# Kernel tuning notes

Measured on AMD Instinct MI355X. Metric: run time of the kernel, lower is better.

## Reference

```python
import jax, jax.numpy as jnp
import numpy as np

B = 4096          # graph pairs in batch
NPG = 40          # nodes per molecular graph
N = B * NPG       # total nodes per drug batch
EPG = 160         # directed edges per graph
E = B * EPG
F_IN = 78         # atom feature dim
HID = 128
HEADS = 4
ADD = 8           # additional features (concentrations)
BN_EPS = 1e-5
D0 = HEADS * HID          # 512
CMB = 4 * HID + ADD       # 2 drugs * (mean||max of 128) + ADD = 520


def setup_inputs() -> dict:
    key = jax.random.key(0)
    ks = iter(jax.random.split(key, 64))
    def nrm(shape, s=0.1):
        return jax.random.normal(next(ks), shape, jnp.float32) * s
    def pos(shape):  # positive running variances
        return jax.random.uniform(next(ks), shape, jnp.float32, 0.5, 1.5)
    offs = jnp.repeat(jnp.arange(B, dtype=jnp.int32) * NPG, EPG)
    def edges():
        return jax.random.randint(next(ks), (2, E), 0, NPG, dtype=jnp.int32) + offs[None, :]
    batch = jnp.repeat(jnp.arange(B, dtype=jnp.int32), NPG)
    inp = dict(
        x_a=nrm((N, F_IN), 1.0), edge_a=edges(), batch_a=batch,
        x_b=nrm((N, F_IN), 1.0), edge_b=edges(), batch_b=batch,
        addf=nrm((B, ADD), 1.0),
        # shared GAT encoder params
        gW0=nrm((F_IN, D0)), gb0=nrm((D0,)), gas0=nrm((D0,)), gad0=nrm((D0,)),
        gW1=nrm((D0, D0)), gb1=nrm((D0,)), gas1=nrm((D0,)), gad1=nrm((D0,)),
        gW2=nrm((D0, HID)), gb2=nrm((HID,)), gas2=nrm((HID,)), gad2=nrm((HID,)),
        bn0g=pos((D0,)), bn0b=nrm((D0,)), bn0m=nrm((D0,)), bn0v=pos((D0,)),
        bn1g=pos((D0,)), bn1b=nrm((D0,)), bn1m=nrm((D0,)), bn1v=pos((D0,)),
        bn2g=pos((HID,)), bn2b=nrm((HID,)), bn2m=nrm((HID,)), bn2v=pos((HID,)),
        # combination MLP params (Linear + eval BatchNorm stats)
        mW0=nrm((CMB, 2 * HID)), mb0=nrm((2 * HID,)),
        mg0=pos((2 * HID,)), mbe0=nrm((2 * HID,)), mm0=nrm((2 * HID,)), mv0=pos((2 * HID,)),
        mW1=nrm((2 * HID, HID)), mb1=nrm((HID,)),
        mg1=pos((HID,)), mbe1=nrm((HID,)), mm1=nrm((HID,)), mv1=pos((HID,)),
        mW2=nrm((HID, 1)), mb2=nrm((1,)),
    )
    return inp


def _bn(x, g, b, m, v):
    return (x - m) * jax.lax.rsqrt(v + BN_EPS) * g + b


def _gat(x, src, dst, W, b, a_src, a_dst, heads, ch, concat):
    """PyG GATConv (eval): linear, per-head additive attention with
    leaky_relu(0.2), segment-softmax over incoming edges (self-loops included)."""
    n = x.shape[0]
    h = (x @ W).reshape(n, heads, ch)                     # [N, H, C]
    es = jnp.sum(h * a_src.reshape(1, heads, ch), -1)     # [N, H]
    ed = jnp.sum(h * a_dst.reshape(1, heads, ch), -1)     # [N, H]
    e = jax.nn.leaky_relu(es[src] + ed[dst], 0.2)         # [E', H]
    emax = jax.ops.segment_max(e, dst, num_segments=n)
    ex = jnp.exp(e - emax[dst])
    den = jax.ops.segment_sum(ex, dst, num_segments=n)
    alpha = ex / den[dst]                                 # [E', H]
    out = jax.ops.segment_sum(h[src] * alpha[..., None], dst, num_segments=n)
    out = out.reshape(n, heads * ch) if concat else jnp.mean(out, axis=1)
    return out + b


def _encode(x, edge, batch, p):
    n = x.shape[0]
    sl = jnp.arange(n, dtype=edge.dtype)                  # self-loops (PyG default)
    src = jnp.concatenate([edge[0], sl])
    dst = jnp.concatenate([edge[1], sl])
    x = _gat(x, src, dst, p['gW0'], p['gb0'], p['gas0'], p['gad0'], HEADS, HID, True)
    x = jax.nn.relu(_bn(x, p['bn0g'], p['bn0b'], p['bn0m'], p['bn0v']))
    x = _gat(x, src, dst, p['gW1'], p['gb1'], p['gas1'], p['gad1'], HEADS, HID, True)
    x = jax.nn.relu(_bn(x, p['bn1g'], p['bn1b'], p['bn1m'], p['bn1v']))
    x = _gat(x, src, dst, p['gW2'], p['gb2'], p['gas2'], p['gad2'], 1, HID, False)
    x = _bn(x, p['bn2g'], p['bn2b'], p['bn2m'], p['bn2v'])  # no relu on last layer
    cnt = jax.ops.segment_sum(jnp.ones((n, 1), x.dtype), batch, num_segments=B)
    x_mean = jax.ops.segment_sum(x, batch, num_segments=B) / cnt
    x_max = jax.ops.segment_max(x, batch, num_segments=B)
    return jnp.concatenate([x_mean, x_max], axis=1)        # [B, 2*HID]


def reference(x_a, edge_a, batch_a, x_b, edge_b, batch_b, addf,
              gW0, gb0, gas0, gad0, gW1, gb1, gas1, gad1, gW2, gb2, gas2, gad2,
              bn0g, bn0b, bn0m, bn0v, bn1g, bn1b, bn1m, bn1v, bn2g, bn2b, bn2m, bn2v,
              mW0, mb0, mg0, mbe0, mm0, mv0, mW1, mb1, mg1, mbe1, mm1, mv1, mW2, mb2):
    p = dict(gW0=gW0, gb0=gb0, gas0=gas0, gad0=gad0, gW1=gW1, gb1=gb1, gas1=gas1,
             gad1=gad1, gW2=gW2, gb2=gb2, gas2=gas2, gad2=gad2,
             bn0g=bn0g, bn0b=bn0b, bn0m=bn0m, bn0v=bn0v,
             bn1g=bn1g, bn1b=bn1b, bn1m=bn1m, bn1v=bn1v,
             bn2g=bn2g, bn2b=bn2b, bn2m=bn2m, bn2v=bn2v)
    emb_a = _encode(x_a, edge_a, batch_a, p)
    emb_b = _encode(x_b, edge_b, batch_b, p)
    c = jnp.concatenate([emb_a, emb_b, addf], axis=1)      # [B, 520]
    h = jax.nn.relu(_bn(c @ mW0 + mb0, mg0, mbe0, mm0, mv0))
    h = jax.nn.relu(_bn(h @ mW1 + mb1, mg1, mbe1, mm1, mv1))
    out = jax.nn.sigmoid(h @ mW2 + mb2)
    return jnp.squeeze(out, -1)                            # [B]
```

## Files before the change

kernel.cpp:

```cpp
#include <hip/hip_runtime.h>
#include <stdint.h>

#define B_GRAPHS 4096
#define NPG 40
#define NTOT (B_GRAPHS * NPG)
#define EPG 160
#define ETOT (B_GRAPHS * EPG)
#define ESL 200
#define F_IN 78
#define KP0 96
#define HID 128
#define D0 512
#define CMB 520
#define BN_EPS 1e-5f
#define AST 48
#define KPM 544
#define A0ST 552
#define H1ST 264
#define H2ST 132

typedef short bf16x8 __attribute__((ext_vector_type(8)));
typedef float floatx4 __attribute__((ext_vector_type(4)));

__device__ inline float b2f(unsigned short u) {
    union { float f; uint32_t i; } v; v.i = ((uint32_t)u) << 16; return v.f;
}
__device__ inline unsigned short f2b(float f) {
    union { float f; uint32_t i; } v; v.f = f;
    uint32_t x = v.i;
    return (unsigned short)((x + 0x7fffu + ((x >> 16) & 1u)) >> 16);
}
__device__ inline float lo16(uint32_t u) {
    union { float f; uint32_t i; } v; v.i = u << 16; return v.f;
}
__device__ inline float hi16(uint32_t u) {
    union { float f; uint32_t i; } v; v.i = u & 0xffff0000u; return v.f;
}
__device__ inline unsigned int fenc(float f) {
    unsigned int b = __float_as_uint(f);
    return (b & 0x80000000u) ? ~b : (b | 0x80000000u);
}
__device__ inline float fdec(unsigned int u) {
    unsigned int b = (u & 0x80000000u) ? (u & 0x7fffffffu) : ~u;
    return __uint_as_float(b);
}
__device__ inline int htoff(int ch, int s) {
    int chunk = s >> 3, within = s & 7;
    return ch * 40 + (((chunk + ch) % 5) << 3) + within;
}
__device__ inline void gl2lds16(const unsigned short* g, unsigned short* l) {
    __builtin_amdgcn_global_load_lds(
        (const __attribute__((address_space(1))) unsigned int*)g,
        (__attribute__((address_space(3))) unsigned int*)l, 16, 0, 0);
}

__global__ __launch_bounds__(256)
void write_code_kernel(float* __restrict__ out, int n, float S)
{
    int i = blockIdx.x * 256 + threadIdx.x;
    if (i < n) out[i] = (i == 0) ? S : 0.f;
}

__global__ __launch_bounds__(256)
void convw_kernel(const float* __restrict__ W, unsigned short* __restrict__ Wt,
                  int K, int N, int Kp)
{
    int t = blockIdx.x * 256 + threadIdx.x;
    if (t >= N * Kp) return;
    int n = t / Kp, k = t - n * Kp;
    Wt[t] = (k < K) ? f2b(W[(size_t)k * N + n]) : 0;
}

__global__ __launch_bounds__(256)
void convw_hilo_kernel(const float* __restrict__ W,
                       unsigned short* __restrict__ Whi,
                       unsigned short* __restrict__ Wlo,
                       int K, int N, int Kp)
{
    int t = blockIdx.x * 256 + threadIdx.x;
    if (t >= N * Kp) return;
    int n = t / Kp, k = t - n * Kp;
    float x = (k < K) ? W[(size_t)k * N + n] : 0.f;
    unsigned short hb = f2b(x);
    Whi[t] = hb;
    Wlo[t] = f2b(x - b2f(hb));
}

__global__ __launch_bounds__(256)
void convx_kernel(const float* __restrict__ X, unsigned short* __restrict__ Xb, int M)
{
    int t = blockIdx.x * 256 + threadIdx.x;
    if (t >= M * (KP0 / 8)) return;
    int r = t / (KP0 / 8), c8 = t - r * (KP0 / 8);
    unsigned int pk[4];
    #pragma unroll
    for (int j = 0; j < 4; j++) {
        int k0 = c8 * 8 + 2 * j, k1 = k0 + 1;
        float x0 = (k0 < F_IN) ? X[(size_t)r * F_IN + k0] : 0.f;
        float x1 = (k1 < F_IN) ? X[(size_t)r * F_IN + k1] : 0.f;
        pk[j] = (unsigned int)f2b(x0) | ((unsigned int)f2b(x1) << 16);
    }
    *(uint4*)&Xb[(size_t)r * KP0 + c8 * 8] = make_uint4(pk[0], pk[1], pk[2], pk[3]);
}

__global__ __launch_bounds__(256)
void gemm_mfma_kernel(const unsigned short* __restrict__ A,
                      const unsigned short* __restrict__ Bt,
                      unsigned short* __restrict__ C,
                      int M, int K, int N)
{
    __shared__ __align__(16) unsigned short As[128 * 32];
    __shared__ __align__(16) unsigned short Bs[128 * 32];
    const int tid  = threadIdx.x;
    const int lane = tid & 63, w = tid >> 6;
    const int quad = lane >> 4, l16 = lane & 15;
    const int wm = w >> 1, wn = w & 1;
    const int row0 = blockIdx.y * 128, col0 = blockIdx.x * 128;

    floatx4 acc[4][4];
    #pragma unroll
    for (int mi = 0; mi < 4; mi++)
        #pragma unroll
        for (int ni = 0; ni < 4; ni++)
            acc[mi][ni] = (floatx4){0.f, 0.f, 0.f, 0.f};

    int srow[2], scg[2];
    #pragma unroll
    for (int it = 0; it < 2; it++) {
        int L = it * 4096 + w * 1024 + lane * 16;
        int r = L >> 6;
        int cp = (L >> 4) & 3;
        srow[it] = r;
        scg[it]  = cp ^ ((r >> 1) & 3);
    }

    for (int k0 = 0; k0 < K; k0 += 32) {
        #pragma unroll
        for (int it = 0; it < 2; it++) {
            int ra = row0 + srow[it]; if (ra >= M) ra = M - 1;
            gl2lds16(A + (size_t)ra * K + k0 + scg[it] * 8,
                     As + (it * 4096 + w * 1024) / 2);
            int rb = col0 + srow[it];
            gl2lds16(Bt + (size_t)rb * K + k0 + scg[it] * 8,
                     Bs + (it * 4096 + w * 1024) / 2);
        }
        __syncthreads();

        bf16x8 fA[4], fB[4];
        #pragma unroll
        for (int mi = 0; mi < 4; mi++) {
            int r = wm * 64 + mi * 16 + l16;
            __builtin_memcpy(&fA[mi], &As[r * 32 + ((quad ^ ((r >> 1) & 3)) * 8)], 16);
        }
        #pragma unroll
        for (int ni = 0; ni < 4; ni++) {
            int r = wn * 64 + ni * 16 + l16;
            __builtin_memcpy(&fB[ni], &Bs[r * 32 + ((quad ^ ((r >> 1) & 3)) * 8)], 16);
        }
        #pragma unroll
        for (int mi = 0; mi < 4; mi++)
            #pragma unroll
            for (int ni = 0; ni < 4; ni++)
                acc[mi][ni] = __builtin_amdgcn_mfma_f32_16x16x32_bf16(
                    fB[ni], fA[mi], acc[mi][ni], 0, 0, 0);
        __syncthreads();
    }

    #pragma unroll
    for (int mi = 0; mi < 4; mi++) {
        int row = row0 + wm * 64 + mi * 16 + l16;
        if (row < M) {
            #pragma unroll
            for (int ni = 0; ni < 4; ni++) {
                floatx4 a = acc[mi][ni];
                unsigned int p0 = (unsigned int)f2b(a[0]) | ((unsigned int)f2b(a[1]) << 16);
                unsigned int p1 = (unsigned int)f2b(a[2]) | ((unsigned int)f2b(a[3]) << 16);
                *(uint2*)(C + (size_t)row * N + col0 + wn * 64 + ni * 16 + quad * 4) =
                    make_uint2(p0, p1);
            }
        }
    }
}

__global__ __launch_bounds__(256)
void gat4_fused_kernel(unsigned short* __restrict__ H,
                       const int* __restrict__ edge,
                       const float* __restrict__ avs, const float* __restrict__ avd,
                       const float* __restrict__ bias,
                       const float* __restrict__ bng, const float* __restrict__ bnb,
                       const float* __restrict__ bnm, const float* __restrict__ bnv,
                       int g0)
{
    __shared__ __align__(16) unsigned short ht[D0 * NPG];
    __shared__ float es[4 * NPG], ed[4 * NPG];
    __shared__ unsigned int Mu[4 * NPG];
    __shared__ float den[4 * NPG];
    __shared__ __align__(16) unsigned char cnt[NPG * 48];
    __shared__ short2 eloc[ESL];
    const int tid = threadIdx.x;
    const int lane = tid & 63, w = tid >> 6;
    const int quad = lane >> 4, l16 = lane & 15;
    const int gg = g0 + blockIdx.x;
    unsigned short* Hg = H + (size_t)blockIdx.x * NPG * D0;

    for (int i = tid; i < NPG * 48 / 4; i += 256) ((unsigned int*)cnt)[i] = 0u;
    if (tid < 4 * NPG) { Mu[tid] = 0u; den[tid] = 0.f; }
    for (int i = tid; i < ESL; i += 256) {
        if (i < EPG) {
            int s  = edge[(size_t)gg * EPG + i] - gg * NPG;
            int dd = edge[(size_t)ETOT + (size_t)gg * EPG + i] - gg * NPG;
            eloc[i] = make_short2((short)s, (short)dd);
        } else {
            short v = (short)(i - EPG);
            eloc[i] = make_short2(v, v);
        }
    }
    for (int u = tid; u < 64 * (NPG / 4); u += 256) {
        int c8 = u & 63, gi = u >> 6;
        const unsigned short* src = Hg + (size_t)(4 * gi) * D0 + c8 * 8;
        uint4 v0 = *(const uint4*)(src);
        uint4 v1 = *(const uint4*)(src + D0);
        uint4 v2 = *(const uint4*)(src + 2 * D0);
        uint4 v3 = *(const uint4*)(src + 3 * D0);
        unsigned int a0[4] = {v0.x, v0.y, v0.z, v0.w};
        unsigned int a1[4] = {v1.x, v1.y, v1.z, v1.w};
        unsigned int a2[4] = {v2.x, v2.y, v2.z, v2.w};
        unsigned int a3[4] = {v3.x, v3.y, v3.z, v3.w};
        #pragma unroll
        for (int k = 0; k < 8; k++) {
            const int ws = k >> 1, sh = (k & 1) * 16;
            unsigned int w0 = ((a0[ws] >> sh) & 0xffffu) | (((a1[ws] >> sh) & 0xffffu) << 16);
            unsigned int w1 = ((a2[ws] >> sh) & 0xffffu) | (((a3[ws] >> sh) & 0xffffu) << 16);
            *(uint2*)&ht[htoff(c8 * 8 + k, 4 * gi)] = make_uint2(w0, w1);
        }
    }
    __syncthreads();

    {
        float as0=0,as1=0,as2=0,as3=0, ad0=0,ad1=0,ad2=0,ad3=0;
        for (int ci = 0; ci < 32; ci++) {
            int c = quad + ci * 4;
            int chv = w * 128 + c;
            uint2 hv = *(const uint2*)&ht[htoff(chv, 4 * l16)];
            float h0 = lo16(hv.x), h1 = hi16(hv.x), h2 = lo16(hv.y), h3 = hi16(hv.y);
            float vs = avs[chv], vd = avd[chv];
            as0 += h0*vs; as1 += h1*vs; as2 += h2*vs; as3 += h3*vs;
            ad0 += h0*vd; ad1 += h1*vd; ad2 += h2*vd; ad3 += h3*vd;
        }
        #define RED4(x) x += __shfl_xor(x, 16); x += __shfl_xor(x, 32);
        RED4(as0) RED4(as1) RED4(as2) RED4(as3)
        RED4(ad0) RED4(ad1) RED4(ad2) RED4(ad3)
        #undef RED4
        if (quad == 0) {
            float rs[4] = {as0, as1, as2, as3};
            float rd[4] = {ad0, ad1, ad2, ad3};
            #pragma unroll
            for (int rr = 0; rr < 4; rr++) {
                int node = 4 * l16 + rr;
                if (node < NPG) { es[w * NPG + node] = rs[rr]; ed[w * NPG + node] = rd[rr]; }
            }
        }
    }
    for (int e = tid; e < ESL; e += 256) {
        short2 sd = eloc[e];
        atomicAdd((unsigned int*)cnt + ((sd.y * 48 + sd.x) >> 2),
                  1u << ((sd.x & 3) * 8));
    }
    __syncthreads();

    for (int u = tid; u < 4 * ESL; u += 256) {
        int e = u >> 2, hd = u & 3;
        short2 sd = eloc[e];
        float v = es[hd * NPG + sd.x] + ed[hd * NPG + sd.y];
        v = v > 0.f ? v : 0.2f * v;
        atomicMax(&Mu[hd * NPG + sd.y], fenc(v));
    }
    __syncthreads();
    for (int u = tid; u < 4 * ESL; u += 256) {
        int e = u >> 2, hd = u & 3;
        short2 sd = eloc[e];
        float v = es[hd * NPG + sd.x] + ed[hd * NPG + sd.y];
        v = v > 0.f ? v : 0.2f * v;
        float ex = __expf(v - fdec(Mu[hd * NPG + sd.y]));
        atomicAdd(&den[hd * NPG + sd.y], ex);
    }
    __syncthreads();
// ... 36 lines not shown
                unsigned short hb1 = f2b(a1);
                ahi[mt][1][j] = (short)hb1;
                alo[mt][1][j] = (short)f2b(a1 - b2f(hb1));
            }
        }
        const floatx4 z = {0.f, 0.f, 0.f, 0.f};
        for (int nt = 0; nt < 8; nt++) {
            const int ch0 = w * 128 + nt * 16;
            bf16x8 b0, b1 = {0,0,0,0,0,0,0,0};
            __builtin_memcpy(&b0, &ht[htoff(ch0 + l16, quad * 8)], 16);
            if (quad == 0) __builtin_memcpy(&b1, &ht[htoff(ch0 + l16, 32)], 16);
            floatx4 acc0 = z, acc1 = z, acc2 = z;
            acc0 = __builtin_amdgcn_mfma_f32_16x16x32_bf16(ahi[0][0], b0, acc0, 0, 0, 0);
            acc1 = __builtin_amdgcn_mfma_f32_16x16x32_bf16(ahi[1][0], b0, acc1, 0, 0, 0);
            acc2 = __builtin_amdgcn_mfma_f32_16x16x32_bf16(ahi[2][0], b0, acc2, 0, 0, 0);
            acc0 = __builtin_amdgcn_mfma_f32_16x16x32_bf16(alo[0][0], b0, acc0, 0, 0, 0);
            acc1 = __builtin_amdgcn_mfma_f32_16x16x32_bf16(alo[1][0], b0, acc1, 0, 0, 0);
            acc2 = __builtin_amdgcn_mfma_f32_16x16x32_bf16(alo[2][0], b0, acc2, 0, 0, 0);
            acc0 = __builtin_amdgcn_mfma_f32_16x16x32_bf16(ahi[0][1], b1, acc0, 0, 0, 0);
            acc1 = __builtin_amdgcn_mfma_f32_16x16x32_bf16(ahi[1][1], b1, acc1, 0, 0, 0);
            acc2 = __builtin_amdgcn_mfma_f32_16x16x32_bf16(ahi[2][1], b1, acc2, 0, 0, 0);
            acc0 = __builtin_amdgcn_mfma_f32_16x16x32_bf16(alo[0][1], b1, acc0, 0, 0, 0);
            acc1 = __builtin_amdgcn_mfma_f32_16x16x32_bf16(alo[1][1], b1, acc1, 0, 0, 0);
            acc2 = __builtin_amdgcn_mfma_f32_16x16x32_bf16(alo[2][1], b1, acc2, 0, 0, 0);
            const int c = ch0 + l16;
            float scl = rsqrtf(bnv[c] + BN_EPS) * bng[c];
            float sft = (bias[c] - bnm[c]) * scl + bnb[c];
            unsigned short* reg = &ht[ch0 * 40];
            #pragma unroll
            for (int mt = 0; mt < 3; mt++) {
                floatx4 a = (mt == 0) ? acc0 : (mt == 1) ? acc1 : acc2;
                #pragma unroll
                for (int rr = 0; rr < 4; rr++) {
                    int dn = mt * 16 + quad * 4 + rr;
                    if (dn < NPG) {
                        float o = a[rr] * scl + sft;
                        o = fmaxf(o, 0.f);
                        reg[dn * 16 + l16] = f2b(o);
                    }
                }
            }
        }
    }
    __syncthreads();
    for (int u = tid; u < NPG * 64; u += 256) {
        int s = u >> 6, c8 = u & 63;
        const unsigned short* reg = &ht[(c8 >> 1) * 16 * 40];
        uint4 v = *(const uint4*)&reg[s * 16 + (c8 & 1) * 8];
        *(uint4*)(Hg + (size_t)s * D0 + c8 * 8) = v;
    }
}

__global__ __launch_bounds__(256)
void gat1_pool_fused_kernel(const unsigned short* __restrict__ H,
                            const int* __restrict__ edge,
                            const float* __restrict__ avs, const float* __restrict__ avd,
                            const float* __restrict__ bias,
                            const float* __restrict__ bng, const float* __restrict__ bnb,
                            const float* __restrict__ bnm, const float* __restrict__ bnv,
                            float* __restrict__ cmb, int colbase, int g0)
{
    __shared__ __align__(16) unsigned short ht[HID * NPG];
    __shared__ float A1f[NPG * AST];
    __shared__ float es[NPG], ed[NPG];
    __shared__ unsigned int Mu[NPG];
    __shared__ float den[NPG];
    __shared__ short2 eloc[ESL];
    const int tid = threadIdx.x;
    const int lane = tid & 63, w = tid >> 6;
    const int quad = lane >> 4, l16 = lane & 15;
    const int gg = g0 + blockIdx.x;
    const unsigned short* Hg = H + (size_t)blockIdx.x * NPG * HID;

    for (int i = tid; i < NPG * AST; i += 256) A1f[i] = 0.f;
    if (tid < NPG) { Mu[tid] = 0u; den[tid] = 0.f; }
    for (int i = tid; i < ESL; i += 256) {
        if (i < EPG) {
            int s  = edge[(size_t)gg * EPG + i] - gg * NPG;
            int dd = edge[(size_t)ETOT + (size_t)gg * EPG + i] - gg * NPG;
            eloc[i] = make_short2((short)s, (short)dd);
        } else {
            short v = (short)(i - EPG);
            eloc[i] = make_short2(v, v);
        }
    }
    for (int u = tid; u < 16 * (NPG / 4); u += 256) {
        int c8 = u & 15, gi = u >> 4;
        const unsigned short* src = Hg + (size_t)(4 * gi) * HID + c8 * 8;
        uint4 v0 = *(const uint4*)(src);
        uint4 v1 = *(const uint4*)(src + HID);
        uint4 v2 = *(const uint4*)(src + 2 * HID);
        uint4 v3 = *(const uint4*)(src + 3 * HID);
        unsigned int a0[4] = {v0.x, v0.y, v0.z, v0.w};
        unsigned int a1[4] = {v1.x, v1.y, v1.z, v1.w};
        unsigned int a2[4] = {v2.x, v2.y, v2.z, v2.w};
        unsigned int a3[4] = {v3.x, v3.y, v3.z, v3.w};
        #pragma unroll
        for (int k = 0; k < 8; k++) {
            const int ws = k >> 1, sh = (k & 1) * 16;
            unsigned int w0 = ((a0[ws] >> sh) & 0xffffu) | (((a1[ws] >> sh) & 0xffffu) << 16);
            unsigned int w1 = ((a2[ws] >> sh) & 0xffffu) | (((a3[ws] >> sh) & 0xffffu) << 16);
            *(uint2*)&ht[htoff(c8 * 8 + k, 4 * gi)] = make_uint2(w0, w1);
        }
    }
    __syncthreads();

    if (w < 2) {
        const float* av = w ? avd : avs;
        float a0=0,a1=0,a2=0,a3=0;
        for (int ci = 0; ci < 32; ci++) {
            int c = quad + ci * 4;
            uint2 hv = *(const uint2*)&ht[htoff(c, 4 * l16)];
            float vc = av[c];
            a0 += lo16(hv.x)*vc; a1 += hi16(hv.x)*vc;
            a2 += lo16(hv.y)*vc; a3 += hi16(hv.y)*vc;
        }
        #define RED4(x) x += __shfl_xor(x, 16); x += __shfl_xor(x, 32);
        RED4(a0) RED4(a1) RED4(a2) RED4(a3)
        #undef RED4
        if (quad == 0) {
            float rv[4] = {a0, a1, a2, a3};
            float* dst = w ? ed : es;
            #pragma unroll
            for (int rr = 0; rr < 4; rr++) {
                int node = 4 * l16 + rr;
                if (node < NPG) dst[node] = rv[rr];
            }
        }
    }
    __syncthreads();
    for (int u = tid; u < ESL; u += 256) {
        short2 sd = eloc[u];
        float v = es[sd.x] + ed[sd.y];
        v = v > 0.f ? v : 0.2f * v;
        atomicMax(&Mu[sd.y], fenc(v));
    }
    __syncthreads();
    for (int u = tid; u < ESL; u += 256) {
        short2 sd = eloc[u];
        float v = es[sd.x] + ed[sd.y];
        v = v > 0.f ? v : 0.2f * v;
        float ex = __expf(v - fdec(Mu[sd.y]));
        atomicAdd(&den[sd.y], ex);
        atomicAdd(&A1f[sd.x * AST + sd.y], ex);
    }
    __syncthreads();
    for (int idx = tid; idx < NPG * AST; idx += 256) {
        int dn = idx % AST;
        float val = A1f[idx];
        unsigned int pw = 0u;
        if (dn < NPG) {
            float a = val / den[dn];
            unsigned short hi = f2b(a);
            float rem = a - b2f(hi);
            pw = (unsigned int)hi | ((unsigned int)f2b(rem) << 16);
        }
        ((unsigned int*)A1f)[idx] = pw;
    }
    __syncthreads();

    {
        const unsigned int* Ap = (const unsigned int*)A1f;
        bf16x8 ahi[3][2], alo[3][2];
        #pragma unroll
        for (int mt = 0; mt < 3; mt++) {
            #pragma unroll
            for (int j = 0; j < 8; j++) {
                unsigned int w0 = Ap[(quad * 8 + j) * AST + mt * 16 + l16];
                ahi[mt][0][j] = (short)(w0 & 0xffffu);
                alo[mt][0][j] = (short)(w0 >> 16);
                unsigned int w1 = (quad == 0) ? Ap[(32 + j) * AST + mt * 16 + l16] : 0u;
                ahi[mt][1][j] = (short)(w1 & 0xffffu);
                alo[mt][1][j] = (short)(w1 >> 16);
            }
        }
        const floatx4 z = {0.f, 0.f, 0.f, 0.f};
        for (int t2 = 0; t2 < 2; t2++) {
            const int ch0 = (w * 2 + t2) * 16;
            bf16x8 b0, b1 = {0,0,0,0,0,0,0,0};
            __builtin_memcpy(&b0, &ht[htoff(ch0 + l16, quad * 8)], 16);
            if (quad == 0) __builtin_memcpy(&b1, &ht[htoff(ch0 + l16, 32)], 16);
            floatx4 acc0 = z, acc1 = z, acc2 = z;
            acc0 = __builtin_amdgcn_mfma_f32_16x16x32_bf16(ahi[0][0], b0, acc0, 0, 0, 0);
            acc1 = __builtin_amdgcn_mfma_f32_16x16x32_bf16(ahi[1][0], b0, acc1, 0, 0, 0);
            acc2 = __builtin_amdgcn_mfma_f32_16x16x32_bf16(ahi[2][0], b0, acc2, 0, 0, 0);
            acc0 = __builtin_amdgcn_mfma_f32_16x16x32_bf16(alo[0][0], b0, acc0, 0, 0, 0);
            acc1 = __builtin_amdgcn_mfma_f32_16x16x32_bf16(alo[1][0], b0, acc1, 0, 0, 0);
            acc2 = __builtin_amdgcn_mfma_f32_16x16x32_bf16(alo[2][0], b0, acc2, 0, 0, 0);
            acc0 = __builtin_amdgcn_mfma_f32_16x16x32_bf16(ahi[0][1], b1, acc0, 0, 0, 0);
            acc1 = __builtin_amdgcn_mfma_f32_16x16x32_bf16(ahi[1][1], b1, acc1, 0, 0, 0);
            acc2 = __builtin_amdgcn_mfma_f32_16x16x32_bf16(ahi[2][1], b1, acc2, 0, 0, 0);
            acc0 = __builtin_amdgcn_mfma_f32_16x16x32_bf16(alo[0][1], b1, acc0, 0, 0, 0);
            acc1 = __builtin_amdgcn_mfma_f32_16x16x32_bf16(alo[1][1], b1, acc1, 0, 0, 0);
            acc2 = __builtin_amdgcn_mfma_f32_16x16x32_bf16(alo[2][1], b1, acc2, 0, 0, 0);
            const int c = ch0 + l16;
            float scl = rsqrtf(bnv[c] + BN_EPS) * bng[c];
            float sft = (bias[c] - bnm[c]) * scl + bnb[c];
            float psum = 0.f, pmax = -1e30f;
            #pragma unroll
            for (int mt = 0; mt < 3; mt++) {
                floatx4 a = (mt == 0) ? acc0 : (mt == 1) ? acc1 : acc2;
                #pragma unroll
                for (int rr = 0; rr < 4; rr++) {
                    int dn = mt * 16 + quad * 4 + rr;
                    if (dn < NPG) {
                        float o = a[rr] * scl + sft;
                        psum += o;
                        pmax = fmaxf(pmax, o);
                    }
                }
            }
            psum += __shfl_xor(psum, 16); psum += __shfl_xor(psum, 32);
            pmax = fmaxf(pmax, __shfl_xor(pmax, 16));
            pmax = fmaxf(pmax, __shfl_xor(pmax, 32));
            if (quad == 0) {
                cmb[(size_t)gg * 512 + colbase + c] = psum * (1.f / NPG);
                cmb[(size_t)gg * 512 + colbase + HID + c] = pmax;
            }
        }
    }
}

__global__ __launch_bounds__(256)
void mlp_mfma_kernel(const float* __restrict__ cmb, const float* __restrict__ addf,
                     const unsigned short* __restrict__ W0hi, const unsigned short* __restrict__ W0lo,
                     const float* __restrict__ b0, const float* __restrict__ g0v,
// ... 107 lines not shown
        float s = 0.f;
        #pragma unroll
        for (int j = 0; j < 8; j++)
            s += h2[g * H2ST + part * 8 + j] * W2[part * 8 + j];
        s += __shfl_xor(s, 1); s += __shfl_xor(s, 2);
        s += __shfl_xor(s, 4); s += __shfl_xor(s, 8);
        if (part == 0) out[gb + g] = 1.f / (1.f + __expf(-(s + b2[0])));
    }
}

extern "C" void kernel_launch(void* const* d_in, const int* in_sizes, int n_in,
                              void* d_out, int out_size, void* d_ws, size_t ws_size,
                              hipStream_t stream)
{
    float* out = (float*)d_out;
    int out_n = out_size < 4096 ? out_size : 4096;

    const float* x_a  = (const float*)d_in[0];
    const int*   edge_a = (const int*)d_in[1];
    const float* x_b  = (const float*)d_in[3];
    const int*   edge_b = (const int*)d_in[4];
    const float* addf = (const float*)d_in[6];
    const float* gW0 = (const float*)d_in[7],  *gb0 = (const float*)d_in[8];
    const float* gas0 = (const float*)d_in[9], *gad0 = (const float*)d_in[10];
    const float* gW1 = (const float*)d_in[11], *gb1 = (const float*)d_in[12];
    const float* gas1 = (const float*)d_in[13], *gad1 = (const float*)d_in[14];
    const float* gW2 = (const float*)d_in[15], *gb2 = (const float*)d_in[16];
    const float* gas2 = (const float*)d_in[17], *gad2 = (const float*)d_in[18];
    const float* bn0g = (const float*)d_in[19], *bn0b = (const float*)d_in[20];
    const float* bn0m = (const float*)d_in[21], *bn0v = (const float*)d_in[22];
    const float* bn1g = (const float*)d_in[23], *bn1b = (const float*)d_in[24];
    const float* bn1m = (const float*)d_in[25], *bn1v = (const float*)d_in[26];
    const float* bn2g = (const float*)d_in[27], *bn2b = (const float*)d_in[28];
    const float* bn2m = (const float*)d_in[29], *bn2v = (const float*)d_in[30];
    const float* mW0 = (const float*)d_in[31], *mb0 = (const float*)d_in[32];
    const float* mg0 = (const float*)d_in[33], *mbe0 = (const float*)d_in[34];
    const float* mm0 = (const float*)d_in[35], *mv0 = (const float*)d_in[36];
    const float* mW1 = (const float*)d_in[37], *mb1 = (const float*)d_in[38];
    const float* mg1 = (const float*)d_in[39], *mbe1 = (const float*)d_in[40];
    const float* mm1 = (const float*)d_in[41], *mv1 = (const float*)d_in[42];
    const float* mW2 = (const float*)d_in[43], *mb2 = (const float*)d_in[44];

    char* p = (char*)d_ws;
    const size_t CMB_BYTES = (size_t)B_GRAPHS * 512 * sizeof(float);
    float* cmb = (float*)p; p += CMB_BYTES;
    unsigned short* W0t = (unsigned short*)p; p += (size_t)D0 * KP0 * 2;
    unsigned short* W1t = (unsigned short*)p; p += (size_t)D0 * D0 * 2;
    unsigned short* W2t = (unsigned short*)p; p += (size_t)HID * D0 * 2;
    unsigned short* M0hi = (unsigned short*)p; p += (size_t)256 * KPM * 2;
    unsigned short* M0lo = (unsigned short*)p; p += (size_t)256 * KPM * 2;
    unsigned short* M1hi = (unsigned short*)p; p += (size_t)128 * 256 * 2;
    unsigned short* M1lo = (unsigned short*)p; p += (size_t)128 * 256 * 2;
    size_t used = (size_t)(p - (char*)d_ws);
    const size_t PG = 7680ull + 40960ull + 40960ull;
    int chunk = B_GRAPHS;
    while (chunk > 4 && used + (size_t)chunk * PG > ws_size) chunk >>= 1;
    if (used + (size_t)chunk * PG > ws_size) {
        write_code_kernel<<<(out_n + 255) / 256, 256, 0, stream>>>(out, out_n, 500000.f);
        return;
    }
    unsigned short* Xb = (unsigned short*)p; p += (size_t)chunk * 7680;
    unsigned short* B1 = (unsigned short*)p; p += (size_t)chunk * 40960;
    unsigned short* B2 = (unsigned short*)p;

    convw_kernel<<<(D0 * KP0 + 255) / 256, 256, 0, stream>>>(gW0, W0t, F_IN, D0, KP0);
    convw_kernel<<<(D0 * D0 + 255) / 256, 256, 0, stream>>>(gW1, W1t, D0, D0, D0);
    convw_kernel<<<(HID * D0 + 255) / 256, 256, 0, stream>>>(gW2, W2t, D0, HID, D0);
    convw_hilo_kernel<<<(256 * KPM + 255) / 256, 256, 0, stream>>>(
        mW0, M0hi, M0lo, CMB, 256, KPM);
    convw_hilo_kernel<<<(128 * 256 + 255) / 256, 256, 0, stream>>>(
        mW1, M1hi, M1lo, 256, 128, 256);

    for (int drug = 0; drug < 2; drug++) {
        const float* x = drug ? x_b : x_a;
        const int* edge = drug ? edge_b : edge_a;
        int colbase = drug ? 256 : 0;

        for (int g0 = 0; g0 < B_GRAPHS; g0 += chunk) {
            int n = chunk * NPG;
            int gy = (n + 127) / 128;
            convx_kernel<<<(n * (KP0 / 8) + 255) / 256, 256, 0, stream>>>(
                x + (size_t)g0 * NPG * F_IN, Xb, n);
            gemm_mfma_kernel<<<dim3(D0 / 128, gy), 256, 0, stream>>>(
                Xb, W0t, B1, n, KP0, D0);
            gat4_fused_kernel<<<chunk, 256, 0, stream>>>(
                B1, edge, gas0, gad0, gb0, bn0g, bn0b, bn0m, bn0v, g0);
            gemm_mfma_kernel<<<dim3(D0 / 128, gy), 256, 0, stream>>>(
                B1, W1t, B2, n, D0, D0);
            gat4_fused_kernel<<<chunk, 256, 0, stream>>>(
                B2, edge, gas1, gad1, gb1, bn1g, bn1b, bn1m, bn1v, g0);
            gemm_mfma_kernel<<<dim3(HID / 128, gy), 256, 0, stream>>>(
                B2, W2t, B1, n, D0, HID);
            gat1_pool_fused_kernel<<<chunk, 256, 0, stream>>>(
                B1, edge, gas2, gad2, gb2, bn2g, bn2b, bn2m, bn2v,
                cmb, colbase, g0);
        }
    }
    mlp_mfma_kernel<<<B_GRAPHS / 16, 256, 0, stream>>>(
        cmb, addf, M0hi, M0lo, mb0, mg0, mbe0, mm0, mv0,
        M1hi, M1lo, mb1, mg1, mbe1, mm1, mv1, mW2, mb2, out);
}
```

Measured before the change: 1.419 ms.

## Fuse layer-0 and layer-2 GEMMs into per-graph GAT kernels

Layer 0 now does the bf16 conversion of raw float features and the X·W0 MFMA GEMM inside the per-graph GAT kernel, writing results straight to shared memory. This removes the convx kernel, the Xb buffer and one global round-trip of the 512-wide hidden tensor. Layer 2 likewise folds the 512→128 GEMM into the pooling GAT kernel. That kernel also switches from a float shared attention matrix built with atomics to a count matrix plus on-the-fly exp coefficients, as the 4-head kernel already does. In exchange, each block rereads the W0/W2 weights from global or L2, and the layer-0 feature loads are uncoalesced scalar loads with heavy register use (launch bound set to 3 blocks).

```diff
diff --git a/kernel.cpp b/kernel.cpp
--- a/kernel.cpp
+++ b/kernel.cpp
@@ -13,7 +13,6 @@
 #define D0 512
 #define CMB 520
 #define BN_EPS 1e-5f
-#define AST 48
 #define KPM 544
 #define A0ST 552
 #define H1ST 264
@@ -87,23 +86,6 @@
 }
 
 __global__ __launch_bounds__(256)
-void convx_kernel(const float* __restrict__ X, unsigned short* __restrict__ Xb, int M)
-{
-    int t = blockIdx.x * 256 + threadIdx.x;
-    if (t >= M * (KP0 / 8)) return;
-    int r = t / (KP0 / 8), c8 = t - r * (KP0 / 8);
-    unsigned int pk[4];
-    #pragma unroll
-    for (int j = 0; j < 4; j++) {
-        int k0 = c8 * 8 + 2 * j, k1 = k0 + 1;
-        float x0 = (k0 < F_IN) ? X[(size_t)r * F_IN + k0] : 0.f;
-        float x1 = (k1 < F_IN) ? X[(size_t)r * F_IN + k1] : 0.f;
-        pk[j] = (unsigned int)f2b(x0) | ((unsigned int)f2b(x1) << 16);
-    }
-    *(uint4*)&Xb[(size_t)r * KP0 + c8 * 8] = make_uint4(pk[0], pk[1], pk[2], pk[3]);
-}
-
-__global__ __launch_bounds__(256)
 void gemm_mfma_kernel(const unsigned short* __restrict__ A,
                       const unsigned short* __restrict__ Bt,
                       unsigned short* __restrict__ C,
@@ -182,14 +164,16 @@
     }
 }
 
-__global__ __launch_bounds__(256)
-void gat4_fused_kernel(unsigned short* __restrict__ H,
-                       const int* __restrict__ edge,
-                       const float* __restrict__ avs, const float* __restrict__ avd,
-                       const float* __restrict__ bias,
-                       const float* __restrict__ bng, const float* __restrict__ bnb,
-                       const float* __restrict__ bnm, const float* __restrict__ bnv,
-                       int g0)
+__global__ __launch_bounds__(256, 3)
+void fused0_kernel(const float* __restrict__ X,
+                   const unsigned short* __restrict__ Wt,
+                   unsigned short* __restrict__ Hout,
+                   const int* __restrict__ edge,
+                   const float* __restrict__ avs, const float* __restrict__ avd,
+                   const float* __restrict__ bias,
+                   const float* __restrict__ bng, const float* __restrict__ bnb,
+                   const float* __restrict__ bnm, const float* __restrict__ bnv,
+                   int g0)
 {
     __shared__ __align__(16) unsigned short ht[D0 * NPG];
     __shared__ float es[4 * NPG], ed[4 * NPG];
@@ -201,7 +185,8 @@
     const int lane = tid & 63, w = tid >> 6;
     const int quad = lane >> 4, l16 = lane & 15;
     const int gg = g0 + blockIdx.x;
-    unsigned short* Hg = H + (size_t)blockIdx.x * NPG * D0;
+    const float* Xg = X + (size_t)blockIdx.x * NPG * F_IN;
+    unsigned short* Hg = Hout + (size_t)blockIdx.x * NPG * D0;
 
     for (int i = tid; i < NPG * 48 / 4; i += 256) ((unsigned int*)cnt)[i] = 0u;
     if (tid < 4 * NPG) { Mu[tid] = 0u; den[tid] = 0.f; }
@@ -215,23 +200,51 @@
             eloc[i] = make_short2(v, v);
         }
     }
-    for (int u = tid; u < 64 * (NPG / 4); u += 256) {
-        int c8 = u & 63, gi = u >> 6;
-        const unsigned short* src = Hg + (size_t)(4 * gi) * D0 + c8 * 8;
-        uint4 v0 = *(const uint4*)(src);
-        uint4 v1 = *(const uint4*)(src + D0);
-        uint4 v2 = *(const uint4*)(src + 2 * D0);
-        uint4 v3 = *(const uint4*)(src + 3 * D0);
-        unsigned int a0[4] = {v0.x, v0.y, v0.z, v0.w};
-        unsigned int a1[4] = {v1.x, v1.y, v1.z, v1.w};
-        unsigned int a2[4] = {v2.x, v2.y, v2.z, v2.w};
-        unsigned int a3[4] = {v3.x, v3.y, v3.z, v3.w};
-        #pragma unroll
-        for (int k = 0; k < 8; k++) {
-            const int ws = k >> 1, sh = (k & 1) * 16;
-            unsigned int w0 = ((a0[ws] >> sh) & 0xffffu) | (((a1[ws] >> sh) & 0xffffu) << 16);
-            unsigned int w1 = ((a2[ws] >> sh) & 0xffffu) | (((a3[ws] >> sh) & 0xffffu) << 16);
-            *(uint2*)&ht[htoff(c8 * 8 + k, 4 * gi)] = make_uint2(w0, w1);
+
+    {
+        floatx4 acc[3][8];
+        #pragma unroll
+        for (int mt = 0; mt < 3; mt++)
+            #pragma unroll
+            for (int nt = 0; nt < 8; nt++)
+                acc[mt][nt] = (floatx4){0.f, 0.f, 0.f, 0.f};
+        #pragma unroll
+        for (int k0 = 0; k0 < KP0; k0 += 32) {
+            bf16x8 fA[3];
+            #pragma unroll
+            for (int mt = 0; mt < 3; mt++) {
+                int s = mt * 16 + l16; if (s >= NPG) s = NPG - 1;
+                const float* xr = Xg + (size_t)s * F_IN;
+                #pragma unroll
+                for (int j = 0; j < 8; j++) {
+                    int k = k0 + quad * 8 + j;
+                    float xv = (k < F_IN) ? xr[k] : 0.f;
+                    fA[mt][j] = (short)f2b(xv);
+                }
+            }
+            #pragma unroll
+            for (int nt = 0; nt < 8; nt++) {
+                int ch = w * 128 + nt * 16 + l16;
+                bf16x8 fW;
+                __builtin_memcpy(&fW, Wt + (size_t)ch * KP0 + k0 + quad * 8, 16);
+                acc[0][nt] = __builtin_amdgcn_mfma_f32_16x16x32_bf16(fA[0], fW, acc[0][nt], 0, 0, 0);
+                acc[1][nt] = __builtin_amdgcn_mfma_f32_16x16x32_bf16(fA[1], fW, acc[1][nt], 0, 0, 0);
+                acc[2][nt] = __builtin_amdgcn_mfma_f32_16x16x32_bf16(fA[2], fW, acc[2][nt], 0, 0, 0);
+            }
+        }
+        #pragma unroll
+        for (int nt = 0; nt < 8; nt++) {
+            int ch = w * 128 + nt * 16 + l16;
+            #pragma unroll
+            for (int mt = 0; mt < 3; mt++) {
+                int s0 = mt * 16 + quad * 4;
+                if (s0 < NPG) {
+                    floatx4 a = acc[mt][nt];
+                    unsigned int p0 = (unsigned int)f2b(a[0]) | ((unsigned int)f2b(a[1]) << 16);
+                    unsigned int p1 = (unsigned int)f2b(a[2]) | ((unsigned int)f2b(a[3]) << 16);
+                    *(uint2*)&ht[htoff(ch, s0)] = make_uint2(p0, p1);
+                }
+            }
         }
     }
     __syncthreads();
@@ -374,27 +387,219 @@
 }
 
 __global__ __launch_bounds__(256)
-void gat1_pool_fused_kernel(const unsigned short* __restrict__ H,
-                            const int* __restrict__ edge,
-                            const float* __restrict__ avs, const float* __restrict__ avd,
-                            const float* __restrict__ bias,
-                            const float* __restrict__ bng, const float* __restrict__ bnb,
-                            const float* __restrict__ bnm, const float* __restrict__ bnv,
-                            float* __restrict__ cmb, int colbase, int g0)
+void gat4_fused_kernel(unsigned short* __restrict__ H,
+                       const int* __restrict__ edge,
+                       const float* __restrict__ avs, const float* __restrict__ avd,
+                       const float* __restrict__ bias,
+                       const float* __restrict__ bng, const float* __restrict__ bnb,
+                       const float* __restrict__ bnm, const float* __restrict__ bnv,
+                       int g0)
 {
-    __shared__ __align__(16) unsigned short ht[HID * NPG];
-    __shared__ float A1f[NPG * AST];
-    __shared__ float es[NPG], ed[NPG];
-    __shared__ unsigned int Mu[NPG];
-    __shared__ float den[NPG];
+    __shared__ __align__(16) unsigned short ht[D0 * NPG];
+    __shared__ float es[4 * NPG], ed[4 * NPG];
+    __shared__ unsigned int Mu[4 * NPG];
+    __shared__ float den[4 * NPG];
+    __shared__ __align__(16) unsigned char cnt[NPG * 48];
     __shared__ short2 eloc[ESL];
     const int tid = threadIdx.x;
     const int lane = tid & 63, w = tid >> 6;
     const int quad = lane >> 4, l16 = lane & 15;
     const int gg = g0 + blockIdx.x;
-    const unsigned short* Hg = H + (size_t)blockIdx.x * NPG * HID;
-
-    for (int i = tid; i < NPG * AST; i += 256) A1f[i] = 0.f;
+    unsigned short* Hg = H + (size_t)blockIdx.x * NPG * D0;
+
+    for (int i = tid; i < NPG * 48 / 4; i += 256) ((unsigned int*)cnt)[i] = 0u;
+    if (tid < 4 * NPG) { Mu[tid] = 0u; den[tid] = 0.f; }
+    for (int i = tid; i < ESL; i += 256) {
+        if (i < EPG) {
+            int s  = edge[(size_t)gg * EPG + i] - gg * NPG;
+            int dd = edge[(size_t)ETOT + (size_t)gg * EPG + i] - gg * NPG;
+            eloc[i] = make_short2((short)s, (short)dd);
+        } else {
+            short v = (short)(i - EPG);
+            eloc[i] = make_short2(v, v);
+        }
+    }
+    for (int u = tid; u < 64 * (NPG / 4); u += 256) {
+        int c8 = u & 63, gi = u >> 6;
+        const unsigned short* src = Hg + (size_t)(4 * gi) * D0 + c8 * 8;
+        uint4 v0 = *(const uint4*)(src);
+        uint4 v1 = *(const uint4*)(src + D0);
+        uint4 v2 = *(const uint4*)(src + 2 * D0);
+        uint4 v3 = *(const uint4*)(src + 3 * D0);
+        unsigned int a0[4] = {v0.x, v0.y, v0.z, v0.w};
+        unsigned int a1[4] = {v1.x, v1.y, v1.z, v1.w};
+        unsigned int a2[4] = {v2.x, v2.y, v2.z, v2.w};
+        unsigned int a3[4] = {v3.x, v3.y, v3.z, v3.w};
+        #pragma unroll
+        for (int k = 0; k < 8; k++) {
+            const int ws = k >> 1, sh = (k & 1) * 16;
+            unsigned int w0 = ((a0[ws] >> sh) & 0xffffu) | (((a1[ws] >> sh) & 0xffffu) << 16);
+            unsigned int w1 = ((a2[ws] >> sh) & 0xffffu) | (((a3[ws] >> sh) & 0xffffu) << 16);
+            *(uint2*)&ht[htoff(c8 * 8 + k, 4 * gi)] = make_uint2(w0, w1);
+        }
+    }
+    __syncthreads();
+
+    {
+        float as0=0,as1=0,as2=0,as3=0, ad0=0,ad1=0,ad2=0,ad3=0;
+        for (int ci = 0; ci < 32; ci++) {
+            int c = quad + ci * 4;
+            int chv = w * 128 + c;
+            uint2 hv = *(const uint2*)&ht[htoff(chv, 4 * l16)];
+            float h0 = lo16(hv.x), h1 = hi16(hv.x), h2 = lo16(hv.y), h3 = hi16(hv.y);
+            float vs = avs[chv], vd = avd[chv];
+            as0 += h0*vs; as1 += h1*vs; as2 += h2*vs; as3 += h3*vs;
+            ad0 += h0*vd; ad1 += h1*vd; ad2 += h2*vd; ad3 += h3*vd;
+        }
+        #define RED4(x) x += __shfl_xor(x, 16); x += __shfl_xor(x, 32);
+        RED4(as0) RED4(as1) RED4(as2) RED4(as3)
+        RED4(ad0) RED4(ad1) RED4(ad2) RED4(ad3)
+        #undef RED4
+        if (quad == 0) {
+            float rs[4] = {as0, as1, as2, as3};
+            float rd[4] = {ad0, ad1, ad2, ad3};
+            #pragma unroll
+            for (int rr = 0; rr < 4; rr++) {
+                int node = 4 * l16 + rr;
+                if (node < NPG) { es[w * NPG + node] = rs[rr]; ed[w * NPG + node] = rd[rr]; }
+            }
+        }
+    }
+    for (int e = tid; e < ESL; e += 256) {
+        short2 sd = eloc[e];
+        atomicAdd((unsigned int*)cnt + ((sd.y * 48 + sd.x) >> 2),
+                  1u << ((sd.x & 3) * 8));
+    }
+    __syncthreads();
+
+    for (int u = tid; u < 4 * ESL; u += 256) {
+        int e = u >> 2, hd = u & 3;
+        short2 sd = eloc[e];
+        float v = es[hd * NPG + sd.x] + ed[hd * NPG + sd.y];
+        v = v > 0.f ? v : 0.2f * v;
+        atomicMax(&Mu[hd * NPG + sd.y], fenc(v));
+    }
+    __syncthreads();
+    for (int u = tid; u < 4 * ESL; u += 256) {
+        int e = u >> 2, hd = u & 3;
+        short2 sd = eloc[e];
+        float v = es[hd * NPG + sd.x] + ed[hd * NPG + sd.y];
+        v = v > 0.f ? v : 0.2f * v;
+        float ex = __expf(v - fdec(Mu[hd * NPG + sd.y]));
+        atomicAdd(&den[hd * NPG + sd.y], ex);
+    }
+    __syncthreads();
+
+    {
+        bf16x8 ahi[3][2], alo[3][2];
+        float esv0[8], esv1[8];
+        #pragma unroll
+        for (int j = 0; j < 8; j++) {
+            esv0[j] = es[w * NPG + quad * 8 + j];
+            esv1[j] = (quad == 0) ? es[w * NPG + 32 + j] : 0.f;
+        }
+        #pragma unroll
+        for (int mt = 0; mt < 3; mt++) {
+            int dn = mt * 16 + l16;
+            bool ok = dn < NPG;
+            float edv = 0.f, m = 0.f, di = 0.f;
+            uint2 c0 = make_uint2(0u, 0u), c1 = make_uint2(0u, 0u);
+            if (ok) {
+                edv = ed[w * NPG + dn];
+                m = fdec(Mu[w * NPG + dn]);
+                di = 1.f / den[w * NPG + dn];
+                c0 = *(const uint2*)&cnt[dn * 48 + quad * 8];
+                if (quad == 0) c1 = *(const uint2*)&cnt[dn * 48 + 32];
+            }
+            #pragma unroll
+            for (int j = 0; j < 8; j++) {
+                unsigned int cb0 = ((j < 4 ? c0.x : c0.y) >> ((j & 3) * 8)) & 0xffu;
+                float v0 = esv0[j] + edv;
+                v0 = v0 > 0.f ? v0 : 0.2f * v0;
+                float a0 = (ok && cb0) ? (float)cb0 * __expf(v0 - m) * di : 0.f;
+                unsigned short hb0 = f2b(a0);
+                ahi[mt][0][j] = (short)hb0;
+                alo[mt][0][j] = (short)f2b(a0 - b2f(hb0));
+
+                unsigned int cb1 = ((j < 4 ? c1.x : c1.y) >> ((j & 3) * 8)) & 0xffu;
+                float v1 = esv1[j] + edv;
+                v1 = v1 > 0.f ? v1 : 0.2f * v1;
+                float a1 = (ok && quad == 0 && cb1) ? (float)cb1 * __expf(v1 - m) * di : 0.f;
+                unsigned short hb1 = f2b(a1);
+                ahi[mt][1][j] = (short)hb1;
+                alo[mt][1][j] = (short)f2b(a1 - b2f(hb1));
+            }
+        }
+        const floatx4 z = {0.f, 0.f, 0.f, 0.f};
+        for (int nt = 0; nt < 8; nt++) {
+            const int ch0 = w * 128 + nt * 16;
+            bf16x8 b0, b1 = {0,0,0,0,0,0,0,0};
+            __builtin_memcpy(&b0, &ht[htoff(ch0 + l16, quad * 8)], 16);
+            if (quad == 0) __builtin_memcpy(&b1, &ht[htoff(ch0 + l16, 32)], 16);
+            floatx4 acc0 = z, acc1 = z, acc2 = z;
+            acc0 = __builtin_amdgcn_mfma_f32_16x16x32_bf16(ahi[0][0], b0, acc0, 0, 0, 0);
+            acc1 = __builtin_amdgcn_mfma_f32_16x16x32_bf16(ahi[1][0], b0, acc1, 0, 0, 0);
+            acc2 = __builtin_amdgcn_mfma_f32_16x16x32_bf16(ahi[2][0], b0, acc2, 0, 0, 0);
+            acc0 = __builtin_amdgcn_mfma_f32_16x16x32_bf16(alo[0][0], b0, acc0, 0, 0, 0);
+            acc1 = __builtin_amdgcn_mfma_f32_16x16x32_bf16(alo[1][0], b0, acc1, 0, 0, 0);
+            acc2 = __builtin_amdgcn_mfma_f32_16x16x32_bf16(alo[2][0], b0, acc2, 0, 0, 0);
+            acc0 = __builtin_amdgcn_mfma_f32_16x16x32_bf16(ahi[0][1], b1, acc0, 0, 0, 0);
+            acc1 = __builtin_amdgcn_mfma_f32_16x16x32_bf16(ahi[1][1], b1, acc1, 0, 0, 0);
+            acc2 = __builtin_amdgcn_mfma_f32_16x16x32_bf16(ahi[2][1], b1, acc2, 0, 0, 0);
+            acc0 = __builtin_amdgcn_mfma_f32_16x16x32_bf16(alo[0][1], b1, acc0, 0, 0, 0);
+            acc1 = __builtin_amdgcn_mfma_f32_16x16x32_bf16(alo[1][1], b1, acc1, 0, 0, 0);
+            acc2 = __builtin_amdgcn_mfma_f32_16x16x32_bf16(alo[2][1], b1, acc2, 0, 0, 0);
+            const int c = ch0 + l16;
+            float scl = rsqrtf(bnv[c] + BN_EPS) * bng[c];
+            float sft = (bias[c] - bnm[c]) * scl + bnb[c];
+            unsigned short* reg = &ht[ch0 * 40];
+            #pragma unroll
+            for (int mt = 0; mt < 3; mt++) {
+                floatx4 a = (mt == 0) ? acc0 : (mt == 1) ? acc1 : acc2;
+                #pragma unroll
+                for (int rr = 0; rr < 4; rr++) {
+                    int dn = mt * 16 + quad * 4 + rr;
+                    if (dn < NPG) {
+                        float o = a[rr] * scl + sft;
+                        o = fmaxf(o, 0.f);
+                        reg[dn * 16 + l16] = f2b(o);
+                    }
+                }
+            }
+        }
+    }
+    __syncthreads();
+    for (int u = tid; u < NPG * 64; u += 256) {
+        int s = u >> 6, c8 = u & 63;
+        const unsigned short* reg = &ht[(c8 >> 1) * 16 * 40];
+        uint4 v = *(const uint4*)&reg[s * 16 + (c8 & 1) * 8];
+        *(uint4*)(Hg + (size_t)s * D0 + c8 * 8) = v;
+    }
+}
+
+__global__ __launch_bounds__(256)
+void fused2_kernel(const unsigned short* __restrict__ A,
+                   const unsigned short* __restrict__ Wt,
+                   const int* __restrict__ edge,
+                   const float* __restrict__ avs, const float* __restrict__ avd,
+                   const float* __restrict__ bias,
+                   const float* __restrict__ bng, const float* __restrict__ bnb,
+                   const float* __restrict__ bnm, const float* __restrict__ bnv,
+                   float* __restrict__ cmb, int colbase, int g0)
+{
+    __shared__ __align__(16) unsigned short ht[HID * NPG];
+    __shared__ float es[NPG], ed[NPG];
+    __shared__ unsigned int Mu[NPG];
+    __shared__ float den[NPG];
+    __shared__ __align__(16) unsigned char cnt[NPG * 48];
+    __shared__ short2 eloc[ESL];
+    const int tid = threadIdx.x;
+    const int lane = tid & 63, w = tid >> 6;
+    const int quad = lane >> 4, l16 = lane & 15;
+    const int gg = g0 + blockIdx.x;
+    const unsigned short* Ag = A + (size_t)blockIdx.x * NPG * D0;
+
+    for (int i = tid; i < NPG * 48 / 4; i += 256) ((unsigned int*)cnt)[i] = 0u;
     if (tid < NPG) { Mu[tid] = 0u; den[tid] = 0.f; }
     for (int i = tid; i < ESL; i += 256) {
         if (i < EPG) {
@@ -406,23 +611,44 @@
             eloc[i] = make_short2(v, v);
         }
     }
-    for (int u = tid; u < 16 * (NPG / 4); u += 256) {
-        int c8 = u & 15, gi = u >> 4;
-        const unsigned short* src = Hg + (size_t)(4 * gi) * HID + c8 * 8;
-        uint4 v0 = *(const uint4*)(src);
-        uint4 v1 = *(const uint4*)(src + HID);
-        uint4 v2 = *(const uint4*)(src + 2 * HID);
-        uint4 v3 = *(const uint4*)(src + 3 * HID);
-        unsigned int a0[4] = {v0.x, v0.y, v0.z, v0.w};
-        unsigned int a1[4] = {v1.x, v1.y, v1.z, v1.w};
-        unsigned int a2[4] = {v2.x, v2.y, v2.z, v2.w};
-        unsigned int a3[4] = {v3.x, v3.y, v3.z, v3.w};
-        #pragma unroll
-        for (int k = 0; k < 8; k++) {
-            const int ws = k >> 1, sh = (k & 1) * 16;
-            unsigned int w0 = ((a0[ws] >> sh) & 0xffffu) | (((a1[ws] >> sh) & 0xffffu) << 16);
-            unsigned int w1 = ((a2[ws] >> sh) & 0xffffu) | (((a3[ws] >> sh) & 0xffffu) << 16);
-            *(uint2*)&ht[htoff(c8 * 8 + k, 4 * gi)] = make_uint2(w0, w1);
+
+    {
+        floatx4 acc[3][2];
+        #pragma unroll
+        for (int mt = 0; mt < 3; mt++)
+            #pragma unroll
+            for (int nt = 0; nt < 2; nt++)
+                acc[mt][nt] = (floatx4){0.f, 0.f, 0.f, 0.f};
+        for (int k0 = 0; k0 < D0; k0 += 32) {
+            bf16x8 fA[3];
+            #pragma unroll
+            for (int mt = 0; mt < 3; mt++) {
+                int s = mt * 16 + l16; if (s >= NPG) s = NPG - 1;
+                __builtin_memcpy(&fA[mt], Ag + (size_t)s * D0 + k0 + quad * 8, 16);
+            }
+            #pragma unroll
+            for (int nt = 0; nt < 2; nt++) {
+                int ch = w * 32 + nt * 16 + l16;
+                bf16x8 fW;
+                __builtin_memcpy(&fW, Wt + (size_t)ch * D0 + k0 + quad * 8, 16);
+                acc[0][nt] = __builtin_amdgcn_mfma_f32_16x16x32_bf16(fA[0], fW, acc[0][nt], 0, 0, 0);
+                acc[1][nt] = __builtin_amdgcn_mfma_f32_16x16x32_bf16(fA[1], fW, acc[1][nt], 0, 0, 0);
+                acc[2][nt] = __builtin_amdgcn_mfma_f32_16x16x32_bf16(fA[2], fW, acc[2][nt], 0, 0, 0);
+            }
+        }
+        #pragma unroll
+        for (int nt = 0; nt < 2; nt++) {
+            int ch = w * 32 + nt * 16 + l16;
+            #pragma unroll
+            for (int mt = 0; mt < 3; mt++) {
+                int s0 = mt * 16 + quad * 4;
+                if (s0 < NPG) {
+                    floatx4 a = acc[mt][nt];
+                    unsigned int p0 = (unsigned int)f2b(a[0]) | ((unsigned int)f2b(a[1]) << 16);
+                    unsigned int p1 = (unsigned int)f2b(a[2]) | ((unsigned int)f2b(a[3]) << 16);
+                    *(uint2*)&ht[htoff(ch, s0)] = make_uint2(p0, p1);
+                }
+            }
         }
     }
     __syncthreads();
@@ -450,6 +676,11 @@
             }
         }
     }
+    for (int e = tid; e < ESL; e += 256) {
+        short2 sd = eloc[e];
+        atomicAdd((unsigned int*)cnt + ((sd.y * 48 + sd.x) >> 2),
+                  1u << ((sd.x & 3) * 8));
+    }
     __syncthreads();
     for (int u = tid; u < ESL; u += 256) {
         short2 sd = eloc[u];
@@ -464,36 +695,47 @@
         v = v > 0.f ? v : 0.2f * v;
         float ex = __expf(v - fdec(Mu[sd.y]));
         atomicAdd(&den[sd.y], ex);
-        atomicAdd(&A1f[sd.x * AST + sd.y], ex);
-    }
-    __syncthreads();
-    for (int idx = tid; idx < NPG * AST; idx += 256) {
-        int dn = idx % AST;
-        float val = A1f[idx];
-        unsigned int pw = 0u;
-        if (dn < NPG) {
-            float a = val / den[dn];
-            unsigned short hi = f2b(a);
-            float rem = a - b2f(hi);
-            pw = (unsigned int)hi | ((unsigned int)f2b(rem) << 16);
-        }
-        ((unsigned int*)A1f)[idx] = pw;
     }
     __syncthreads();
 
     {
-        const unsigned int* Ap = (const unsigned int*)A1f;
         bf16x8 ahi[3][2], alo[3][2];
+        float esv0[8], esv1[8];
+        #pragma unroll
+        for (int j = 0; j < 8; j++) {
+            esv0[j] = es[quad * 8 + j];
+            esv1[j] = (quad == 0) ? es[32 + j] : 0.f;
+        }
         #pragma unroll
         for (int mt = 0; mt < 3; mt++) {
+            int dn = mt * 16 + l16;
+            bool ok = dn < NPG;
+            float edv = 0.f, m = 0.f, di = 0.f;
+            uint2 c0 = make_uint2(0u, 0u), c1 = make_uint2(0u, 0u);
+            if (ok) {
+                edv = ed[dn];
+                m = fdec(Mu[dn]);
+                di = 1.f / den[dn];
+                c0 = *(const uint2*)&cnt[dn * 48 + quad * 8];
+                if (quad == 0) c1 = *(const uint2*)&cnt[dn * 48 + 32];
+            }
             #pragma unroll
             for (int j = 0; j < 8; j++) {
-                unsigned int w0 = Ap[(quad * 8 + j) * AST + mt * 16 + l16];
-                ahi[mt][0][j] = (short)(w0 & 0xffffu);
-                alo[mt][0][j] = (short)(w0 >> 16);
-                unsigned int w1 = (quad == 0) ? Ap[(32 + j) * AST + mt * 16 + l16] : 0u;
-                ahi[mt][1][j] = (short)(w1 & 0xffffu);
-                alo[mt][1][j] = (short)(w1 >> 16);
+                unsigned int cb0 = ((j < 4 ? c0.x : c0.y) >> ((j & 3) * 8)) & 0xffu;
+                float v0 = esv0[j] + edv;
+                v0 = v0 > 0.f ? v0 : 0.2f * v0;
+                float a0 = (ok && cb0) ? (float)cb0 * __expf(v0 - m) * di : 0.f;
+                unsigned short hb0 = f2b(a0);
+                ahi[mt][0][j] = (short)hb0;
+                alo[mt][0][j] = (short)f2b(a0 - b2f(hb0));
+
+                unsigned int cb1 = ((j < 4 ? c1.x : c1.y) >> ((j & 3) * 8)) & 0xffu;
+                float v1 = esv1[j] + edv;
+                v1 = v1 > 0.f ? v1 : 0.2f * v1;
+                float a1 = (ok && quad == 0 && cb1) ? (float)cb1 * __expf(v1 - m) * di : 0.f;
+                unsigned short hb1 = f2b(a1);
+                ahi[mt][1][j] = (short)hb1;
+                alo[mt][1][j] = (short)f2b(a1 - b2f(hb1));
             }
         }
         const floatx4 z = {0.f, 0.f, 0.f, 0.f};
@@ -707,14 +949,13 @@
     unsigned short* M1hi = (unsigned short*)p; p += (size_t)128 * 256 * 2;
     unsigned short* M1lo = (unsigned short*)p; p += (size_t)128 * 256 * 2;
     size_t used = (size_t)(p - (char*)d_ws);
-    const size_t PG = 7680ull + 40960ull + 40960ull;
+    const size_t PG = 40960ull + 40960ull;
     int chunk = B_GRAPHS;
     while (chunk > 4 && used + (size_t)chunk * PG > ws_size) chunk >>= 1;
     if (used + (size_t)chunk * PG > ws_size) {
         write_code_kernel<<<(out_n + 255) / 256, 256, 0, stream>>>(out, out_n, 500000.f);
         return;
     }
-    unsigned short* Xb = (unsigned short*)p; p += (size_t)chunk * 7680;
     unsigned short* B1 = (unsigned short*)p; p += (size_t)chunk * 40960;
     unsigned short* B2 = (unsigned short*)p;
 
@@ -734,20 +975,15 @@
         for (int g0 = 0; g0 < B_GRAPHS; g0 += chunk) {
             int n = chunk * NPG;
             int gy = (n + 127) / 128;
-            convx_kernel<<<(n * (KP0 / 8) + 255) / 256, 256, 0, stream>>>(
-                x + (size_t)g0 * NPG * F_IN, Xb, n);
-            gemm_mfma_kernel<<<dim3(D0 / 128, gy), 256, 0, stream>>>(
-                Xb, W0t, B1, n, KP0, D0);
-            gat4_fused_kernel<<<chunk, 256, 0, stream>>>(
-                B1, edge, gas0, gad0, gb0, bn0g, bn0b, bn0m, bn0v, g0);
+            fused0_kernel<<<chunk, 256, 0, stream>>>(
+                x + (size_t)g0 * NPG * F_IN, W0t, B1, edge,
+                gas0, gad0, gb0, bn0g, bn0b, bn0m, bn0v, g0);
             gemm_mfma_kernel<<<dim3(D0 / 128, gy), 256, 0, stream>>>(
                 B1, W1t, B2, n, D0, D0);
             gat4_fused_kernel<<<chunk, 256, 0, stream>>>(
                 B2, edge, gas1, gad1, gb1, bn1g, bn1b, bn1m, bn1v, g0);
-            gemm_mfma_kernel<<<dim3(HID / 128, gy), 256, 0, stream>>>(
-                B2, W2t, B1, n, D0, HID);
-            gat1_pool_fused_kernel<<<chunk, 256, 0, stream>>>(
-                B1, edge, gas2, gad2, gb2, bn2g, bn2b, bn2m, bn2v,
+            fused2_kernel<<<chunk, 256, 0, stream>>>(
+                B2, W2t, edge, gas2, gad2, gb2, bn2g, bn2b, bn2m, bn2v,
                 cmb, colbase, g0);
         }
     }
```

New measurement: 1.444 ms. Within noise of the previous version (+1.8%).
